# Performance work log

Hardware: AMD Instinct MI355X
Metric: run time of the kernel (lower is better)

## Reference

```python
import jax, jax.numpy as jnp
import numpy as np
import math

D_RES, N_HEADS, D_HEAD, D_MLP = 1024, 16, 64, 4096
EPS = 1e-5
IGNORE = -100000.0


def setup_inputs() -> dict:
    key = jax.random.key(0)
    ks = jax.random.split(key, 8)
    std = 0.02
    return {
        "resid_pre": jax.random.normal(ks[0], (2, 2048, D_RES), dtype=jnp.float32),
        "ln1_w": jnp.ones((D_RES,), jnp.float32),
        "ln1_b": jnp.zeros((D_RES,), jnp.float32),
        "W_Q": jax.random.normal(ks[1], (N_HEADS, D_RES, D_HEAD), jnp.float32) * std,
        "b_Q": jnp.zeros((N_HEADS, D_HEAD), jnp.float32),
        "W_K": jax.random.normal(ks[2], (N_HEADS, D_RES, D_HEAD), jnp.float32) * std,
        "b_K": jnp.zeros((N_HEADS, D_HEAD), jnp.float32),
        "W_V": jax.random.normal(ks[3], (N_HEADS, D_RES, D_HEAD), jnp.float32) * std,
        "b_V": jnp.zeros((N_HEADS, D_HEAD), jnp.float32),
        "W_O": jax.random.normal(ks[4], (N_HEADS, D_HEAD, D_RES), jnp.float32) * std,
        "b_O": jnp.zeros((D_RES,), jnp.float32),
        "ln2_w": jnp.ones((D_RES,), jnp.float32),
        "ln2_b": jnp.zeros((D_RES,), jnp.float32),
        "W_in": jax.random.normal(ks[5], (D_RES, D_MLP), jnp.float32) * std,
        "b_in": jnp.zeros((D_MLP,), jnp.float32),
        "W_out": jax.random.normal(ks[6], (D_MLP, D_RES), jnp.float32) * std,
        "b_out": jnp.zeros((D_RES,), jnp.float32),
    }


def _layernorm(x, w, b):
    x = x - jnp.mean(x, axis=-1, keepdims=True)
    scale = jnp.sqrt(jnp.mean(x * x, axis=-1, keepdims=True) + EPS)
    return (x / scale) * w + b


def reference(resid_pre, ln1_w, ln1_b, W_Q, b_Q, W_K, b_K, W_V, b_V, W_O, b_O,
              ln2_w, ln2_b, W_in, b_in, W_out, b_out):
    x = _layernorm(resid_pre, ln1_w, ln1_b)  # [b,s,d]
    q = jnp.einsum('bsd,hde->bshe', x, W_Q) + b_Q
    k = jnp.einsum('bsd,hde->bshe', x, W_K) + b_K
    v = jnp.einsum('bsd,hde->bshe', x, W_V) + b_V
    scores = jnp.einsum('bqhe,bkhe->bhqk', q, k) / math.sqrt(D_HEAD)
    S = scores.shape[-1]
    mask = jnp.triu(jnp.ones((S, S), dtype=bool), k=1)
    scores = jnp.where(mask, IGNORE, scores)
    pattern = jax.nn.softmax(scores, axis=-1)
    z = jnp.einsum('bhqk,bkhe->bqhe', pattern, v)
    attn_out = jnp.einsum('bqhe,hed->bqd', z, W_O) + b_O
    resid_mid = resid_pre + attn_out
    y = _layernorm(resid_mid, ln2_w, ln2_b)
    pre = jnp.einsum('bsd,dm->bsm', y, W_in) + b_in
    post = jax.nn.gelu(pre, approximate=False)
    mlp_out = jnp.einsum('bsm,md->bsd', post, W_out) + b_out
    return resid_mid + mlp_out
```

## Files before the change

### kernel.cpp

```cpp
#include <hip/hip_runtime.h>
#include <cstddef>

typedef unsigned short u16;
using short8 = __attribute__((ext_vector_type(8))) short;
using f32x4  = __attribute__((ext_vector_type(4))) float;

__device__ __forceinline__ float bf2f(u16 u) {
  union { unsigned int i; float f; } v; v.i = ((unsigned int)u) << 16; return v.f;
}
__device__ __forceinline__ u16 f2bf(float f) {
  __bf16 h = (__bf16)f;
  return __builtin_bit_cast(unsigned short, h);
}

__device__ __forceinline__ void load_lds16(const u16* g, u16* l) {
  __builtin_amdgcn_global_load_lds((const __attribute__((address_space(1))) void*)g,
                                   (__attribute__((address_space(3))) void*)l, 16, 0, 0);
}

__global__ __launch_bounds__(256) void transpose_k(const float* __restrict__ in,
                                                   u16* __restrict__ out,
                                                   int R, int C,
                                                   long inB, long outB) {
  __shared__ float tile[32][33];
  long zb = blockIdx.z;
  in  += zb * inB;
  out += zb * outB;
  int c0 = blockIdx.x * 32, r0 = blockIdx.y * 32;
  int tx = threadIdx.x, ty = threadIdx.y;
#pragma unroll
  for (int i = 0; i < 32; i += 8)
    tile[ty + i][tx] = in[(long)(r0 + ty + i) * C + c0 + tx];
  __syncthreads();
#pragma unroll
  for (int i = 0; i < 32; i += 8)
    out[(long)(c0 + ty + i) * R + r0 + tx] = f2bf(tile[tx][ty + i]);
}

__global__ __launch_bounds__(256) void transpose_v_k(const u16* __restrict__ qkv,
                                                     u16* __restrict__ vT) {
  __shared__ u16 tile[32][33];
  int bh = blockIdx.z;
  int b = bh >> 4, h = bh & 15;
  const u16* in = qkv + (size_t)b * 2048 * 3072 + 2048 + h * 64;
  u16* out = vT + (size_t)bh * 64 * 2048;
  int e0 = blockIdx.x * 32, s0 = blockIdx.y * 32;
  int tx = threadIdx.x, ty = threadIdx.y;
#pragma unroll
  for (int i = 0; i < 32; i += 8)
    tile[ty + i][tx] = in[(size_t)(s0 + ty + i) * 3072 + e0 + tx];
  __syncthreads();
#pragma unroll
  for (int i = 0; i < 32; i += 8)
    out[(size_t)(e0 + ty + i) * 2048 + s0 + tx] = tile[tx][ty + i];
}

__global__ void build_qkv_bias(const float* __restrict__ bQ, const float* __restrict__ bK,
                               const float* __restrict__ bV, float* __restrict__ out) {
  int i = blockIdx.x * 256 + threadIdx.x;
  float v;
  if (i < 1024) v = bQ[i];
  else if (i < 2048) v = bK[i - 1024];
  else v = bV[i - 2048];
  out[i] = v;
}

__global__ __launch_bounds__(256) void ln_k(const float* __restrict__ inp,
                                            const float* __restrict__ w,
                                            const float* __restrict__ bias,
                                            u16* __restrict__ out) {
  __shared__ float red[2][4];
  int row = blockIdx.x, t = threadIdx.x;
  int wave = t >> 6, lane = t & 63;
  size_t base = (size_t)row * 1024 + t * 4;
  float4 f = *(const float4*)(inp + base);
  float v[4] = {f.x, f.y, f.z, f.w};
  float s = v[0] + v[1] + v[2] + v[3];
#pragma unroll
  for (int off = 32; off; off >>= 1) s += __shfl_xor(s, off, 64);
  if (lane == 0) red[0][wave] = s;
  __syncthreads();
  float mean = (red[0][0] + red[0][1] + red[0][2] + red[0][3]) * (1.f / 1024.f);
  float c[4]; float sq = 0.f;
#pragma unroll
  for (int j = 0; j < 4; ++j) { c[j] = v[j] - mean; sq += c[j] * c[j]; }
#pragma unroll
  for (int off = 32; off; off >>= 1) sq += __shfl_xor(sq, off, 64);
  if (lane == 0) red[1][wave] = sq;
  __syncthreads();
  float var = (red[1][0] + red[1][1] + red[1][2] + red[1][3]) * (1.f / 1024.f);
  float inv = 1.f / sqrtf(var + 1e-5f);
  float4 wv = *(const float4*)(w + t * 4);
  float4 bv = *(const float4*)(bias + t * 4);
  out[base + 0] = f2bf(c[0] * inv * wv.x + bv.x);
  out[base + 1] = f2bf(c[1] * inv * wv.y + bv.y);
  out[base + 2] = f2bf(c[2] * inv * wv.z + bv.z);
  out[base + 3] = f2bf(c[3] * inv * wv.w + bv.w);
}

template<int TN, bool RESIDF, bool GELU, bool OUTF32>
__global__ __launch_bounds__(256, 2) void gemm_k(const u16* __restrict__ A,
                                                 const u16* __restrict__ BT,
                                                 const float* __restrict__ bias,
                                                 const float* __restrict__ resid,
                                                 void* __restrict__ Cout,
                                                 int M, int N, int K) {
  constexpr int NS = TN / 32;
  __shared__ u16 As[128 * 64];
  __shared__ u16 Bs[TN * 64];
  int n0 = blockIdx.x * TN, m0 = blockIdx.y * 128;
  int t = threadIdx.x;
  int wave = t >> 6, lane = t & 63;
  int wr = wave >> 1, wc = wave & 1;
  int ln16 = lane & 15, quad = lane >> 4;

  f32x4 acc[4][NS];
#pragma unroll
  for (int i = 0; i < 4; ++i)
#pragma unroll
    for (int j = 0; j < NS; ++j) acc[i][j] = (f32x4){0.f, 0.f, 0.f, 0.f};

  int lrow8 = lane >> 3;
  int gseg  = (lane & 7) ^ lrow8;
  const u16* aG = A  + (size_t)(m0 + wave * 8 + lrow8) * K + gseg * 8;
  const u16* bG = BT + (size_t)(n0 + wave * 8 + lrow8) * K + gseg * 8;
  u16* aL = As + wave * 8 * 64;
  u16* bL = Bs + wave * 8 * 64;

  int e = ln16 & 7;
  int arow = wr * 64 + ln16;
  int brow = wc * (TN / 2) + ln16;

  for (int k0 = 0; k0 < K; k0 += 64) {
    __syncthreads();
#pragma unroll
    for (int i = 0; i < 4; ++i)
      load_lds16(aG + (size_t)i * 32 * K + k0, aL + i * 32 * 64);
#pragma unroll
    for (int i = 0; i < TN / 32; ++i)
      load_lds16(bG + (size_t)i * 32 * K + k0, bL + i * 32 * 64);
    __syncthreads();
#pragma unroll
    for (int kk = 0; kk < 2; ++kk) {
      int slot = (kk * 4 + quad) ^ e;
      short8 af[4], bf[NS];
#pragma unroll
      for (int ms = 0; ms < 4; ++ms)
        af[ms] = *(const short8*)&As[(arow + ms * 16) * 64 + slot * 8];
#pragma unroll
      for (int ns = 0; ns < NS; ++ns)
        bf[ns] = *(const short8*)&Bs[(brow + ns * 16) * 64 + slot * 8];
#pragma unroll
      for (int ms = 0; ms < 4; ++ms)
#pragma unroll
        for (int ns = 0; ns < NS; ++ns)
          acc[ms][ns] = __builtin_amdgcn_mfma_f32_16x16x32_bf16(af[ms], bf[ns], acc[ms][ns], 0, 0, 0);
    }
  }

#pragma unroll
  for (int ms = 0; ms < 4; ++ms)
#pragma unroll
    for (int ns = 0; ns < NS; ++ns)
#pragma unroll
      for (int r = 0; r < 4; ++r) {
        int grow = m0 + wr * 64 + ms * 16 + quad * 4 + r;
        int gcol = n0 + wc * (TN / 2) + ns * 16 + ln16;
        size_t idx = (size_t)grow * N + gcol;
        float v = acc[ms][ns][r] + bias[gcol];
        if (GELU) v = 0.5f * v * (1.f + erff(v * 0.70710678118654752f));
        if (RESIDF) v += resid[idx];
        if (OUTF32) ((float*)Cout)[idx] = v;
        else        ((u16*)Cout)[idx] = f2bf(v);
      }
}

__global__ __launch_bounds__(256) void attn_k(const u16* __restrict__ qkv,
                                              const u16* __restrict__ vT,
                                              u16* __restrict__ z) {
  __shared__ u16 Ks[64 * 64];
  __shared__ u16 Vs[64 * 64];
  __shared__ u16 Ps[2][4][16][72];
  int pair = blockIdx.x, h = blockIdx.y, b = blockIdx.z;
  int qtA = pair, qtB = 31 - pair;
  int t = threadIdx.x, wave = t >> 6, lane = t & 63;
  int ln16 = lane & 15, quad = lane >> 4;

  int qbase[2] = {qtA * 64 + wave * 16, qtB * 64 + wave * 16};
  short8 aq[2][2];
#pragma unroll
  for (int i = 0; i < 2; ++i) {
    const u16* qrow = qkv + (size_t)(b * 2048 + qbase[i] + ln16) * 3072 + h * 64;
    aq[i][0] = *(const short8*)(qrow + quad * 8);
    aq[i][1] = *(const short8*)(qrow + 32 + quad * 8);
  }

  f32x4 zero4 = {0.f, 0.f, 0.f, 0.f};
  f32x4 o[2][4];
  float l_i[2][4];
#pragma unroll
  for (int i = 0; i < 2; ++i)
#pragma unroll
    for (int n = 0; n < 4; ++n) { o[i][n] = zero4; l_i[i][n] = 0.f; }

  int lrow = lane >> 3;
  int gseg = (lane & 7) ^ lrow;
  const u16* kB = qkv + (size_t)(b * 2048 + wave * 16 + lrow) * 3072 + 1024 + h * 64 + gseg * 8;
  const u16* vB = vT + ((size_t)(b * 16 + h) * 64 + wave * 16 + lrow) * 2048 + gseg * 8;
  u16* kL = Ks + wave * 16 * 64;
  u16* vL = Vs + wave * 16 * 64;

  int e = ln16 & 7;
  int nkt = qtB + 1;
  for (int kt = 0; kt < nkt; ++kt) {
    __syncthreads();
    size_t kOff = (size_t)kt * 64 * 3072;
    size_t vOff = (size_t)kt * 64;
#pragma unroll
    for (int i = 0; i < 2; ++i) {
      load_lds16(kB + kOff + (size_t)i * 8 * 3072, kL + i * 8 * 64);
      load_lds16(vB + vOff + (size_t)i * 8 * 2048, vL + i * 8 * 64);
    }
    __syncthreads();

    int kg = kt * 64;
#pragma unroll
    for (int i = 0; i < 2; ++i) {
      if (i == 0 && kt > qtA) continue;
      f32x4 s[4] = {zero4, zero4, zero4, zero4};
#pragma unroll
      for (int kk = 0; kk < 2; ++kk) {
        short8 a = aq[i][kk];
        int slot = (kk * 4 + quad) ^ e;
#pragma unroll
        for (int n = 0; n < 4; ++n) {
          short8 kb = *(const short8*)&Ks[(n * 16 + ln16) * 64 + slot * 8];
          s[n] = __builtin_amdgcn_mfma_f32_16x16x32_bf16(a, kb, s[n], 0, 0, 0);
        }
      }
#pragma unroll
      for (int r = 0; r < 4; ++r) {
        int gq = qbase[i] + quad * 4 + r;
        float sum = 0.f;
#pragma unroll
        for (int n = 0; n < 4; ++n) {
          float p = (kg + n * 16 + ln16 > gq) ? 0.f : __expf(s[n][r] * 0.125f);
          sum += p;
          Ps[i][wave][quad * 4 + r][n * 16 + ln16] = f2bf(p);
        }
#pragma unroll
        for (int off = 8; off; off >>= 1) sum += __shfl_xor(sum, off, 16);
        l_i[i][r] += sum;
      }
#pragma unroll
      for (int kk = 0; kk < 2; ++kk) {
        short8 ap = *(const short8*)&Ps[i][wave][ln16][kk * 32 + quad * 8];
        int slot = (kk * 4 + quad) ^ e;
#pragma unroll
        for (int n = 0; n < 4; ++n) {
          short8 bv = *(const short8*)&Vs[(n * 16 + ln16) * 64 + slot * 8];
          o[i][n] = __builtin_amdgcn_mfma_f32_16x16x32_bf16(ap, bv, o[i][n], 0, 0, 0);
        }
      }
    }
  }

#pragma unroll
  for (int i = 0; i < 2; ++i) {
    float inv[4];
#pragma unroll
    for (int r = 0; r < 4; ++r) inv[r] = 1.f / l_i[i][r];
#pragma unroll
    for (int n = 0; n < 4; ++n)
#pragma unroll
      for (int r = 0; r < 4; ++r)
        z[(size_t)(b * 2048 + qbase[i] + quad * 4 + r) * 1024 + h * 64 + n * 16 + ln16] =
            f2bf(o[i][n][r] * inv[r]);
  }
}

extern "C" void kernel_launch(void* const* d_in, const int* in_sizes, int n_in,
                              void* d_out, int out_size, void* d_ws, size_t ws_size,
                              hipStream_t stream) {
  const float* resid_pre = (const float*)d_in[0];
  const float* ln1_w = (const float*)d_in[1];
  const float* ln1_b = (const float*)d_in[2];
  const float* W_Q  = (const float*)d_in[3];
  const float* b_Q  = (const float*)d_in[4];
  const float* W_K  = (const float*)d_in[5];
  const float* b_K  = (const float*)d_in[6];
  const float* W_V  = (const float*)d_in[7];
  const float* b_V  = (const float*)d_in[8];
  const float* W_O  = (const float*)d_in[9];
  const float* b_O  = (const float*)d_in[10];
  const float* ln2_w = (const float*)d_in[11];
  const float* ln2_b = (const float*)d_in[12];
  const float* W_in  = (const float*)d_in[13];
  const float* b_in  = (const float*)d_in[14];
  const float* W_out = (const float*)d_in[15];
  const float* b_out = (const float*)d_in[16];
  float* out = (float*)d_out;

  char* w = (char*)d_ws;
  u16* WqkvT = (u16*)w;  w += (size_t)3072 * 1024 * 2;
  u16* WoT   = (u16*)w;  w += (size_t)1024 * 1024 * 2;
  u16* WinT  = (u16*)w;  w += (size_t)4096 * 1024 * 2;
  u16* WoutT = (u16*)w;  w += (size_t)1024 * 4096 * 2;
  float* qkvBias = (float*)w; w += 3072 * 4;
  u16* xln   = (u16*)w;  w += (size_t)4096 * 1024 * 2;
  float* resid_mid = (float*)w; w += (size_t)4096 * 1024 * 4;
  u16* qkvBuf = (u16*)w; w += (size_t)4096 * 3072 * 2;
  u16* zBuf  = (u16*)w;  w += (size_t)4096 * 1024 * 2;
  u16* vTBuf = (u16*)w;  w += (size_t)32 * 64 * 2048 * 2;
  u16* hBuf  = qkvBuf;

  dim3 tb(32, 8);
  transpose_k<<<dim3(2, 32, 16), tb, 0, stream>>>(W_Q, WqkvT,                1024, 64, 65536, 65536);
  transpose_k<<<dim3(2, 32, 16), tb, 0, stream>>>(W_K, WqkvT + 1024 * 1024,  1024, 64, 65536, 65536);
  transpose_k<<<dim3(2, 32, 16), tb, 0, stream>>>(W_V, WqkvT + 2048 * 1024,  1024, 64, 65536, 65536);
  transpose_k<<<dim3(32, 32, 1), tb, 0, stream>>>(W_O,  WoT,   1024, 1024, 0, 0);
  transpose_k<<<dim3(128, 32, 1), tb, 0, stream>>>(W_in, WinT,  1024, 4096, 0, 0);
  transpose_k<<<dim3(32, 128, 1), tb, 0, stream>>>(W_out, WoutT, 4096, 1024, 0, 0);
  build_qkv_bias<<<12, 256, 0, stream>>>(b_Q, b_K, b_V, qkvBias);

  ln_k<<<4096, 256, 0, stream>>>(resid_pre, ln1_w, ln1_b, xln);
  gemm_k<128, false, false, false><<<dim3(24, 32), 256, 0, stream>>>(
      xln, WqkvT, qkvBias, nullptr, qkvBuf, 4096, 3072, 1024);
  transpose_v_k<<<dim3(2, 64, 32), tb, 0, stream>>>(qkvBuf, vTBuf);
  attn_k<<<dim3(16, 16, 2), 256, 0, stream>>>(qkvBuf, vTBuf, zBuf);
  gemm_k<64, true, false, true><<<dim3(16, 32), 256, 0, stream>>>(
      zBuf, WoT, b_O, resid_pre, resid_mid, 4096, 1024, 1024);
  ln_k<<<4096, 256, 0, stream>>>(resid_mid, ln2_w, ln2_b, xln);
  gemm_k<128, false, true, false><<<dim3(32, 32), 256, 0, stream>>>(
      xln, WinT, b_in, nullptr, hBuf, 4096, 4096, 1024);
  gemm_k<64, true, false, true><<<dim3(16, 32), 256, 0, stream>>>(
      hBuf, WoutT, b_out, resid_mid, out, 4096, 1024, 4096);
}
```

Measured before the change: 362.1 us.

## Split attention blocks to one query tile each instead of paired tiles

The attention kernel stops pairing a short and a long causal query tile per block. Each block now handles a single 64-row query tile, one 16-row slice per wave, and the grid doubles to 32 blocks along the sequence. The goal is more independent blocks and fewer live registers per thread, which should raise occupancy. The cost is an uneven causal workload across blocks and K/V tiles being reloaded by more blocks. exp is also switched to exp2f with a prescaled log2e factor.

Result: slower. 412.5 us (+13.9%).

```diff
diff --git a/kernel.cpp b/kernel.cpp
--- a/kernel.cpp
+++ b/kernel.cpp
@@ -180,28 +180,20 @@
                                               u16* __restrict__ z) {
   __shared__ u16 Ks[64 * 64];
   __shared__ u16 Vs[64 * 64];
-  __shared__ u16 Ps[2][4][16][72];
-  int pair = blockIdx.x, h = blockIdx.y, b = blockIdx.z;
-  int qtA = pair, qtB = 31 - pair;
+  __shared__ u16 Ps[4][16][72];
+  int j = blockIdx.x, h = blockIdx.y, b = blockIdx.z;
   int t = threadIdx.x, wave = t >> 6, lane = t & 63;
   int ln16 = lane & 15, quad = lane >> 4;
-
-  int qbase[2] = {qtA * 64 + wave * 16, qtB * 64 + wave * 16};
-  short8 aq[2][2];
-#pragma unroll
-  for (int i = 0; i < 2; ++i) {
-    const u16* qrow = qkv + (size_t)(b * 2048 + qbase[i] + ln16) * 3072 + h * 64;
-    aq[i][0] = *(const short8*)(qrow + quad * 8);
-    aq[i][1] = *(const short8*)(qrow + 32 + quad * 8);
-  }
+  int qt = j * 4 + wave;
+  int qbase = qt * 16;
+
+  const u16* qrow = qkv + (size_t)(b * 2048 + qbase + ln16) * 3072 + h * 64;
+  short8 aq0 = *(const short8*)(qrow + quad * 8);
+  short8 aq1 = *(const short8*)(qrow + 32 + quad * 8);
 
   f32x4 zero4 = {0.f, 0.f, 0.f, 0.f};
-  f32x4 o[2][4];
-  float l_i[2][4];
-#pragma unroll
-  for (int i = 0; i < 2; ++i)
-#pragma unroll
-    for (int n = 0; n < 4; ++n) { o[i][n] = zero4; l_i[i][n] = 0.f; }
+  f32x4 o[4]; o[0] = zero4; o[1] = zero4; o[2] = zero4; o[3] = zero4;
+  float l_i[4] = {0.f, 0.f, 0.f, 0.f};
 
   int lrow = lane >> 3;
   int gseg = (lane & 7) ^ lrow;
@@ -210,8 +202,9 @@
   u16* kL = Ks + wave * 16 * 64;
   u16* vL = Vs + wave * 16 * 64;
 
+  const float SC = 0.125f * 1.44269504088896340736f;
   int e = ln16 & 7;
-  int nkt = qtB + 1;
+  int nkt = j + 1;
   for (int kt = 0; kt < nkt; ++kt) {
     __syncthreads();
     size_t kOff = (size_t)kt * 64 * 3072;
@@ -224,59 +217,52 @@
     __syncthreads();
 
     int kg = kt * 64;
-#pragma unroll
-    for (int i = 0; i < 2; ++i) {
-      if (i == 0 && kt > qtA) continue;
-      f32x4 s[4] = {zero4, zero4, zero4, zero4};
-#pragma unroll
-      for (int kk = 0; kk < 2; ++kk) {
-        short8 a = aq[i][kk];
-        int slot = (kk * 4 + quad) ^ e;
-#pragma unroll
-        for (int n = 0; n < 4; ++n) {
-          short8 kb = *(const short8*)&Ks[(n * 16 + ln16) * 64 + slot * 8];
-          s[n] = __builtin_amdgcn_mfma_f32_16x16x32_bf16(a, kb, s[n], 0, 0, 0);
-        }
+    f32x4 s[4] = {zero4, zero4, zero4, zero4};
+#pragma unroll
+    for (int kk = 0; kk < 2; ++kk) {
+      short8 a = (kk == 0) ? aq0 : aq1;
+      int slot = (kk * 4 + quad) ^ e;
+#pragma unroll
+      for (int n = 0; n < 4; ++n) {
+        short8 kb = *(const short8*)&Ks[(n * 16 + ln16) * 64 + slot * 8];
+        s[n] = __builtin_amdgcn_mfma_f32_16x16x32_bf16(a, kb, s[n], 0, 0, 0);
       }
-#pragma unroll
-      for (int r = 0; r < 4; ++r) {
-        int gq = qbase[i] + quad * 4 + r;
-        float sum = 0.f;
-#pragma unroll
-        for (int n = 0; n < 4; ++n) {
-          float p = (kg + n * 16 + ln16 > gq) ? 0.f : __expf(s[n][r] * 0.125f);
-          sum += p;
-          Ps[i][wave][quad * 4 + r][n * 16 + ln16] = f2bf(p);
-        }
-#pragma unroll
-        for (int off = 8; off; off >>= 1) sum += __shfl_xor(sum, off, 16);
-        l_i[i][r] += sum;
+    }
+#pragma unroll
+    for (int r = 0; r < 4; ++r) {
+      int gq = qbase + quad * 4 + r;
+      float sum = 0.f;
+#pragma unroll
+      for (int n = 0; n < 4; ++n) {
+        float p = (kg + n * 16 + ln16 > gq) ? 0.f : exp2f(s[n][r] * SC);
+        sum += p;
+        Ps[wave][quad * 4 + r][n * 16 + ln16] = f2bf(p);
       }
 #pragma unroll
-      for (int kk = 0; kk < 2; ++kk) {
-        short8 ap = *(const short8*)&Ps[i][wave][ln16][kk * 32 + quad * 8];
-        int slot = (kk * 4 + quad) ^ e;
-#pragma unroll
-        for (int n = 0; n < 4; ++n) {
-          short8 bv = *(const short8*)&Vs[(n * 16 + ln16) * 64 + slot * 8];
-          o[i][n] = __builtin_amdgcn_mfma_f32_16x16x32_bf16(ap, bv, o[i][n], 0, 0, 0);
-        }
+      for (int off = 8; off; off >>= 1) sum += __shfl_xor(sum, off, 16);
+      l_i[r] += sum;
+    }
+#pragma unroll
+    for (int kk = 0; kk < 2; ++kk) {
+      short8 ap = *(const short8*)&Ps[wave][ln16][kk * 32 + quad * 8];
+      int slot = (kk * 4 + quad) ^ e;
+#pragma unroll
+      for (int n = 0; n < 4; ++n) {
+        short8 bv = *(const short8*)&Vs[(n * 16 + ln16) * 64 + slot * 8];
+        o[n] = __builtin_amdgcn_mfma_f32_16x16x32_bf16(ap, bv, o[n], 0, 0, 0);
       }
     }
   }
 
-#pragma unroll
-  for (int i = 0; i < 2; ++i) {
-    float inv[4];
-#pragma unroll
-    for (int r = 0; r < 4; ++r) inv[r] = 1.f / l_i[i][r];
-#pragma unroll
-    for (int n = 0; n < 4; ++n)
-#pragma unroll
-      for (int r = 0; r < 4; ++r)
-        z[(size_t)(b * 2048 + qbase[i] + quad * 4 + r) * 1024 + h * 64 + n * 16 + ln16] =
-            f2bf(o[i][n][r] * inv[r]);
-  }
+  float inv[4];
+#pragma unroll
+  for (int r = 0; r < 4; ++r) inv[r] = 1.f / l_i[r];
+#pragma unroll
+  for (int n = 0; n < 4; ++n)
+#pragma unroll
+    for (int r = 0; r < 4; ++r)
+      z[(size_t)(b * 2048 + qbase + quad * 4 + r) * 1024 + h * 64 + n * 16 + ln16] =
+          f2bf(o[n][r] * inv[r]);
 }
 
 extern "C" void kernel_launch(void* const* d_in, const int* in_sizes, int n_in,
@@ -327,7 +313,7 @@
   gemm_k<128, false, false, false><<<dim3(24, 32), 256, 0, stream>>>(
       xln, WqkvT, qkvBias, nullptr, qkvBuf, 4096, 3072, 1024);
   transpose_v_k<<<dim3(2, 64, 32), tb, 0, stream>>>(qkvBuf, vTBuf);
-  attn_k<<<dim3(16, 16, 2), 256, 0, stream>>>(qkvBuf, vTBuf, zBuf);
+  attn_k<<<dim3(32, 16, 2), 256, 0, stream>>>(qkvBuf, vTBuf, zBuf);
   gemm_k<64, true, false, true><<<dim3(16, 32), 256, 0, stream>>>(
       zBuf, WoT, b_O, resid_pre, resid_mid, 4096, 1024, 1024);
   ln_k<<<4096, 256, 0, stream>>>(resid_mid, ln2_w, ln2_b, xln);
```
